# Kernel optimization log

Measured on AMD Instinct MI355X. Metric: run time of the kernel, lower is better.

## Reference

```python
import jax, jax.numpy as jnp
import numpy as np

N1 = 50000        # nodes in g1
N_LAYERS = 3
N2 = N1 * N_LAYERS  # nodes in g2 (kron tiling)
E1 = 800000
E2 = 2400000
D = 64
LEAKY_SLOPE = 0.01


def graph_conv(x, src, dst, num_nodes, W, b):
    """DGL GraphConv with norm='both', in_feats == out_feats (aggregate-then-matmul).
    h = D_in^{-1/2} A D_out^{-1/2} x W + b, degrees clamped to >=1.
    """
    ones_e = jnp.ones(src.shape[0], dtype=x.dtype)
    out_deg = jax.ops.segment_sum(ones_e, src, num_segments=num_nodes)
    in_deg = jax.ops.segment_sum(ones_e, dst, num_segments=num_nodes)
    norm_src = jnp.power(jnp.clip(out_deg, 1.0), -0.5)  # [N]
    norm_dst = jnp.power(jnp.clip(in_deg, 1.0), -0.5)   # [N]
    feat = x * norm_src[:, None]                         # [N, D]
    agg = jax.ops.segment_sum(feat[src], dst, num_segments=num_nodes)  # [N, D]
    rst = agg * norm_dst[:, None]
    return rst @ W + b


def setup_inputs() -> dict:
    key = jax.random.key(0)
    k = jax.random.split(key, 8)
    return {
        "node_features": jax.random.normal(k[0], (N1, D), dtype=jnp.float32),
        "WQ": jax.random.normal(k[1], (D, D), dtype=jnp.float32) * (1.0 / np.sqrt(D)),
        "bQ": jnp.zeros((D,), dtype=jnp.float32),
        "WM": jax.random.normal(k[2], (D, D), dtype=jnp.float32) * (1.0 / np.sqrt(D)),
        "bM": jnp.zeros((D,), dtype=jnp.float32),
        "src1": jax.random.randint(k[3], (E1,), 0, N1, dtype=jnp.int32),
        "dst1": jax.random.randint(k[4], (E1,), 0, N1, dtype=jnp.int32),
        "src2": jax.random.randint(k[5], (E2,), 0, N2, dtype=jnp.int32),
        "dst2": jax.random.randint(k[6], (E2,), 0, N2, dtype=jnp.int32),
    }


def reference(node_features, WQ, bQ, WM, bM, src1, dst1, src2, dst2):
    h_Q1 = graph_conv(node_features, src1, dst1, N1, WQ, bQ)
    h_Q1 = jax.nn.leaky_relu(h_Q1, negative_slope=LEAKY_SLOPE)
    # torch.kron(ones(n_layers,1), h_Q1) == vertical tiling
    M_feat = jnp.tile(h_Q1, (N_LAYERS, 1))  # [N_LAYERS*N1, D]
    h_M1 = graph_conv(M_feat, src2, dst2, N2, WM, bM)
    return jax.nn.leaky_relu(h_M1, negative_slope=LEAKY_SLOPE)
```

## Files before the change

### kernel.cpp

```cpp
#include <hip/hip_runtime.h>
#include <hip/hip_fp16.h>

constexpr int cN1 = 50000;
constexpr int cN2 = 150000;
constexpr int cE1 = 800000;
constexpr int cE2 = 2400000;
constexpr int cD  = 64;
constexpr int MAXB = 640;
#define LEAKY 0.01f

constexpr int NB1 = (cN1 + 255) / 256;
constexpr int NB2 = (cN2 + 255) / 256;

constexpr int BD1 = 64, BD2 = 192, BS1 = 64, BS2 = 192, CVB = 256;
constexpr int PR0 = BD1;
constexpr int PR1 = PR0 + BD2;
constexpr int PR2 = PR1 + BS1;
constexpr int PR3 = PR2 + BS2;
constexpr int PR4 = PR3 + CVB;

constexpr int SD1 = 128, SD2 = 384, SS1 = 64, SS2 = 192;

__device__ __forceinline__ void bucket_count_region(
    const int* __restrict__ idx, int E4, int* __restrict__ bcnt, int nbuck,
    int b, int B, int* h) {
    for (int i = threadIdx.x; i < nbuck; i += 256) h[i] = 0;
    __syncthreads();
    const int4* v4 = (const int4*)idx;
    for (int i = b * 256 + threadIdx.x; i < E4; i += B * 256) {
        int4 v = v4[i];
        atomicAdd(&h[v.x >> 8], 1);
        atomicAdd(&h[v.y >> 8], 1);
        atomicAdd(&h[v.z >> 8], 1);
        atomicAdd(&h[v.w >> 8], 1);
    }
    __syncthreads();
    for (int i = threadIdx.x; i < nbuck; i += 256) {
        int c = h[i];
        if (c) atomicAdd(&bcnt[i], c);
    }
}

__global__ __launch_bounds__(256) void prep_kernel(
    const int* __restrict__ dst1, const int* __restrict__ dst2,
    const int* __restrict__ src1, const int* __restrict__ src2,
    const float* __restrict__ x, __half* __restrict__ xh,
    int* __restrict__ bcntD1, int* __restrict__ bcntD2,
    int* __restrict__ bcntS1, int* __restrict__ bcntS2) {
    __shared__ int h[MAXB];
    int b = blockIdx.x;
    if (b < PR0) {
        bucket_count_region(dst1, cE1 / 4, bcntD1, NB1, b, BD1, h);
    } else if (b < PR1) {
        bucket_count_region(dst2, cE2 / 4, bcntD2, NB2, b - PR0, BD2, h);
    } else if (b < PR2) {
        bucket_count_region(src1, cE1 / 4, bcntS1, NB1, b - PR1, BS1, h);
    } else if (b < PR3) {
        bucket_count_region(src2, cE2 / 4, bcntS2, NB2, b - PR2, BS2, h);
    } else {
        int i = (b - PR3) * 256 + threadIdx.x;
        const int n4 = cN1 * cD / 4;
        for (; i < n4; i += CVB * 256) {
            float4 v = ((const float4*)x)[i];
            __half2* o = (__half2*)xh;
            o[2 * i]     = __floats2half2_rn(v.x, v.y);
            o[2 * i + 1] = __floats2half2_rn(v.z, v.w);
        }
    }
}

__global__ __launch_bounds__(256) void scan4_kernel(
    int* __restrict__ bcntD1, int* __restrict__ bbaseD1, int* __restrict__ bcurD1,
    int* __restrict__ bcntD2, int* __restrict__ bbaseD2, int* __restrict__ bcurD2,
    int* __restrict__ bcntS1, int* __restrict__ bbaseS1, int* __restrict__ bcurS1,
    int* __restrict__ bcntS2, int* __restrict__ bbaseS2, int* __restrict__ bcurS2,
    int* __restrict__ offs1, int* __restrict__ offs2) {
    int b = blockIdx.x;
    int tid = threadIdx.x;
    int* bcnt; int* bbase; int* bcur; int n; int e;
    if (b == 0)      { bcnt = bcntD1; bbase = bbaseD1; bcur = bcurD1; n = NB1; e = cE1; }
    else if (b == 1) { bcnt = bcntD2; bbase = bbaseD2; bcur = bcurD2; n = NB2; e = cE2; }
    else if (b == 2) { bcnt = bcntS1; bbase = bbaseS1; bcur = bcurS1; n = NB1; e = cE1; }
    else             { bcnt = bcntS2; bbase = bbaseS2; bcur = bcurS2; n = NB2; e = cE2; }
    if (b == 0 && tid == 0) offs1[cN1] = cE1;
    if (b == 1 && tid == 0) offs2[cN2] = cE2;
    __shared__ int s[256];
    int v[4];
    int t = 0;
#pragma unroll
    for (int j = 0; j < 4; ++j) { int i = tid * 4 + j; v[j] = (i < n) ? bcnt[i] : 0; t += v[j]; }
    s[tid] = t; __syncthreads();
    for (int off = 1; off < 256; off <<= 1) {
        int a = (tid >= off) ? s[tid - off] : 0;
        __syncthreads();
        s[tid] += a;
        __syncthreads();
    }
    int run = s[tid] - t;
#pragma unroll
    for (int j = 0; j < 4; ++j) {
        int i = tid * 4 + j;
        if (i < n) { bbase[i] = run; bcur[i] = run; run += v[j]; }
    }
    if (tid == 0) bbase[n] = e;
}

__global__ __launch_bounds__(256) void scatter4_kernel(
    const int* __restrict__ src1, const int* __restrict__ dst1,
    int* __restrict__ bcurD1, unsigned int* __restrict__ pairs1,
    const int* __restrict__ src2, const int* __restrict__ dst2,
    int* __restrict__ bcurD2, unsigned int* __restrict__ pairs2,
    int* __restrict__ bcurS1, unsigned char* __restrict__ sval1,
    int* __restrict__ bcurS2, unsigned char* __restrict__ sval2) {
    __shared__ int hist[MAXB];
    __shared__ int cur[MAXB];
    int tid = threadIdx.x;
    int bx = blockIdx.x;
    bool pairMode;
    const int* key; const int* pay; int* bcur;
    unsigned int* pout = nullptr; unsigned char* bout = nullptr;
    int nbuck, E, blk, nblk;
    if (bx < SD1) {
        pairMode = true;  key = dst1; pay = src1; bcur = bcurD1; pout = pairs1;
        nbuck = NB1; E = cE1; blk = bx; nblk = SD1;
    } else if (bx < SD1 + SD2) {
        pairMode = true;  key = dst2; pay = src2; bcur = bcurD2; pout = pairs2;
        nbuck = NB2; E = cE2; blk = bx - SD1; nblk = SD2;
    } else if (bx < SD1 + SD2 + SS1) {
        pairMode = false; key = src1; pay = nullptr; bcur = bcurS1; bout = sval1;
        nbuck = NB1; E = cE1; blk = bx - SD1 - SD2; nblk = SS1;
    } else {
        pairMode = false; key = src2; pay = nullptr; bcur = bcurS2; bout = sval2;
        nbuck = NB2; E = cE2; blk = bx - SD1 - SD2 - SS1; nblk = SS2;
    }
    int spe = (((E / 4) + nblk - 1) / nblk) * 4;
    int b0 = blk * spe;
    int b1 = b0 + spe; if (b1 > E) b1 = E;
    for (int i = tid; i < nbuck; i += 256) hist[i] = 0;
    __syncthreads();
    for (int i = b0 + tid * 4; i < b1; i += 1024) {
        int4 d = *(const int4*)(key + i);
        atomicAdd(&hist[d.x >> 8], 1);
        atomicAdd(&hist[d.y >> 8], 1);
        atomicAdd(&hist[d.z >> 8], 1);
        atomicAdd(&hist[d.w >> 8], 1);
    }
    __syncthreads();
    for (int i = tid; i < nbuck; i += 256) cur[i] = atomicAdd(&bcur[i], hist[i]);
    __syncthreads();
    if (pairMode) {
        for (int i = b0 + tid * 4; i < b1; i += 1024) {
            int4 d = *(const int4*)(key + i);
            int4 s = *(const int4*)(pay + i);
            int p0 = atomicAdd(&cur[d.x >> 8], 1);
            pout[p0] = ((unsigned)(d.x & 255) << 24) | (unsigned)s.x;
            int p1 = atomicAdd(&cur[d.y >> 8], 1);
            pout[p1] = ((unsigned)(d.y & 255) << 24) | (unsigned)s.y;
            int p2 = atomicAdd(&cur[d.z >> 8], 1);
            pout[p2] = ((unsigned)(d.z & 255) << 24) | (unsigned)s.z;
            int p3 = atomicAdd(&cur[d.w >> 8], 1);
            pout[p3] = ((unsigned)(d.w & 255) << 24) | (unsigned)s.w;
        }
    } else {
        for (int i = b0 + tid * 4; i < b1; i += 1024) {
            int4 d = *(const int4*)(key + i);
            int p0 = atomicAdd(&cur[d.x >> 8], 1); bout[p0] = (unsigned char)(d.x & 255);
            int p1 = atomicAdd(&cur[d.y >> 8], 1); bout[p1] = (unsigned char)(d.y & 255);
            int p2 = atomicAdd(&cur[d.z >> 8], 1); bout[p2] = (unsigned char)(d.z & 255);
            int p3 = atomicAdd(&cur[d.w >> 8], 1); bout[p3] = (unsigned char)(d.w & 255);
        }
    }
}

__global__ __launch_bounds__(256) void sbin_kernel(
    const unsigned char* __restrict__ sval1, const int* __restrict__ bbaseS1,
    float* __restrict__ nsrc1,
    const unsigned char* __restrict__ sval2, const int* __restrict__ bbaseS2,
    float* __restrict__ nsrc2) {
    const unsigned char* sv; const int* bbase; float* nsrc; int N, bk;
    if (blockIdx.x < NB1) { sv = sval1; bbase = bbaseS1; nsrc = nsrc1; N = cN1; bk = blockIdx.x; }
    else                  { sv = sval2; bbase = bbaseS2; nsrc = nsrc2; N = cN2; bk = blockIdx.x - NB1; }
    __shared__ int cnt[256];
    int tid = threadIdx.x;
    cnt[tid] = 0;
    __syncthreads();
    int k0 = bbase[bk];
    int k1 = bbase[bk + 1];
    for (int k = k0 + tid; k < k1; k += 256) atomicAdd(&cnt[sv[k]], 1);
    __syncthreads();
    int lo = bk << 8;
    int span = N - lo; if (span > 256) span = 256;
    if (tid < span) {
        int d = cnt[tid];
        d = d < 1 ? 1 : d;
        nsrc[lo + tid] = rsqrtf((float)d);
    }
}

__global__ __launch_bounds__(256) void bin12_kernel(
    const unsigned int* __restrict__ pairs1, const int* __restrict__ bbase1,
    const float* __restrict__ nsrc1, unsigned int* __restrict__ sorted1,
    int* __restrict__ offs1,
    const unsigned int* __restrict__ pairs2, const int* __restrict__ bbase2,
    const float* __restrict__ nsrc2, unsigned int* __restrict__ sorted2,
    int* __restrict__ offs2) {
    const unsigned int* pairs; const int* bbase; const float* nsrc;
    unsigned int* sorted; int* offs; int N, foldn, bk;
    if (blockIdx.x < NB1) {
        pairs = pairs1; bbase = bbase1; nsrc = nsrc1; sorted = sorted1;
        offs = offs1; N = cN1; foldn = 0; bk = blockIdx.x;
    } else {
        pairs = pairs2; bbase = bbase2; nsrc = nsrc2; sorted = sorted2;
        offs = offs2; N = cN2; foldn = cN1; bk = blockIdx.x - NB1;
    }
    __shared__ int cnt[256];
    __shared__ int s[256];
    __shared__ int cur[256];
    int tid = threadIdx.x;
    int lo = bk << 8;
    int span = N - lo; if (span > 256) span = 256;
    int k0 = bbase[bk];
    int k1 = bbase[bk + 1];
    cnt[tid] = 0;
    __syncthreads();
    for (int k = k0 + tid; k < k1; k += 256) atomicAdd(&cnt[pairs[k] >> 24], 1);
    __syncthreads();
    int v = cnt[tid];
    s[tid] = v; __syncthreads();
    for (int off = 1; off < 256; off <<= 1) {
        int a = (tid >= off) ? s[tid - off] : 0;
        __syncthreads();
        s[tid] += a;
        __syncthreads();
    }
    int excl = s[tid] - v;
    cur[tid] = k0 + excl;
    if (tid < span) offs[lo + tid] = k0 + excl;
    __syncthreads();
    for (int k = k0 + tid; k < k1; k += 256) {
        unsigned pr = pairs[k];
        int d = pr >> 24;
        int sidx = (int)(pr & 0xFFFFFFu);
        int r = sidx;
        if (foldn) {
            if (r >= 2 * foldn) r -= 2 * foldn;
            else if (r >= foldn) r -= foldn;
        }
        __half nh = __float2half(nsrc[sidx]);
        int pos = atomicAdd(&cur[d], 1);
        sorted[pos] = ((unsigned)__half_as_ushort(nh) << 16) | (unsigned)r;
    }
}

#define FMA8(v, nv)                                                     \
    {                                                                   \
        float2 f0 = __half22float2(*(const __half2*)&(v).x);            \
        float2 f1 = __half22float2(*(const __half2*)&(v).y);            \
        float2 f2 = __half22float2(*(const __half2*)&(v).z);            \
        float2 f3 = __half22float2(*(const __half2*)&(v).w);            \
        a0.x = fmaf(f0.x, nv, a0.x); a0.y = fmaf(f0.y, nv, a0.y);       \
        a0.z = fmaf(f1.x, nv, a0.z); a0.w = fmaf(f1.y, nv, a0.w);       \
        a1.x = fmaf(f2.x, nv, a1.x); a1.y = fmaf(f2.y, nv, a1.y);       \
        a1.z = fmaf(f3.x, nv, a1.z); a1.w = fmaf(f3.y, nv, a1.w);       \
    }

template <bool EPI>
__global__ __launch_bounds__(256) void agg_csr_kernel(
    const __half* __restrict__ feat, const unsigned int* __restrict__ sorted,
    const int* __restrict__ offs, float* __restrict__ outp,
    const float* __restrict__ bias, int N) {
    int w = (blockIdx.x * blockDim.x + threadIdx.x) >> 4;
    if (w >= N) return;
    int l16  = threadIdx.x & 15;
    int slot = l16 >> 3;
    int c    = l16 & 7;

    int k0 = offs[w];
    int k1 = offs[w + 1];
    float4 a0 = {0.f, 0.f, 0.f, 0.f};
    float4 a1 = {0.f, 0.f, 0.f, 0.f};

    int k = k0 + slot;
    for (; k + 2 < k1; k += 4) {
        unsigned eA = sorted[k];
        unsigned eB = sorted[k + 2];
        float nA = __half2float(__ushort_as_half((unsigned short)(eA >> 16)));
        float nB = __half2float(__ushort_as_half((unsigned short)(eB >> 16)));
        int rA = (int)(eA & 0xFFFFu);
        int rB = (int)(eB & 0xFFFFu);
        uint4 vA = *(const uint4*)(feat + (size_t)rA * cD + c * 8);
        uint4 vB = *(const uint4*)(feat + (size_t)rB * cD + c * 8);
        FMA8(vA, nA);
        FMA8(vB, nB);
    }
    if (k < k1) {
        unsigned e = sorted[k];
        float nv = __half2float(__ushort_as_half((unsigned short)(e >> 16)));
        int r = (int)(e & 0xFFFFu);
        uint4 v = *(const uint4*)(feat + (size_t)r * cD + c * 8);
        FMA8(v, nv);
    }

    a0.x += __shfl_xor(a0.x, 8); a0.y += __shfl_xor(a0.y, 8);
    a0.z += __shfl_xor(a0.z, 8); a0.w += __shfl_xor(a0.w, 8);
    a1.x += __shfl_xor(a1.x, 8); a1.y += __shfl_xor(a1.y, 8);
    a1.z += __shfl_xor(a1.z, 8); a1.w += __shfl_xor(a1.w, 8);

    if (slot == 0) {
        if (EPI) {
            int dg = k1 - k0;
            float nd = rsqrtf((float)(dg < 1 ? 1 : dg));
            float4 b0 = *(const float4*)(bias + c * 8);
            float4 b1 = *(const float4*)(bias + c * 8 + 4);
            float4 r0, r1;
            r0.x = fmaf(a0.x, nd, b0.x); r0.y = fmaf(a0.y, nd, b0.y);
            r0.z = fmaf(a0.z, nd, b0.z); r0.w = fmaf(a0.w, nd, b0.w);
            r1.x = fmaf(a1.x, nd, b1.x); r1.y = fmaf(a1.y, nd, b1.y);
            r1.z = fmaf(a1.z, nd, b1.z); r1.w = fmaf(a1.w, nd, b1.w);
            r0.x = r0.x > 0.f ? r0.x : LEAKY * r0.x;
            r0.y = r0.y > 0.f ? r0.y : LEAKY * r0.y;
            r0.z = r0.z > 0.f ? r0.z : LEAKY * r0.z;
            r0.w = r0.w > 0.f ? r0.w : LEAKY * r0.w;
            r1.x = r1.x > 0.f ? r1.x : LEAKY * r1.x;
            r1.y = r1.y > 0.f ? r1.y : LEAKY * r1.y;
            r1.z = r1.z > 0.f ? r1.z : LEAKY * r1.z;
            r1.w = r1.w > 0.f ? r1.w : LEAKY * r1.w;
            *(float4*)(outp + (size_t)w * cD + c * 8) = r0;
            *(float4*)(outp + (size_t)w * cD + c * 8 + 4) = r1;
        } else {
            *(float4*)(outp + (size_t)w * cD + c * 8) = a0;
            *(float4*)(outp + (size_t)w * cD + c * 8 + 4) = a1;
        }
    }
}
#undef FMA8

__global__ __launch_bounds__(256) void gemm12_kernel(
    const float* __restrict__ A, const int* __restrict__ offs,
    const float* __restrict__ WQ_, const float* __restrict__ bQ_,
    const float* __restrict__ WM_, __half* __restrict__ g, int N) {
    __shared__ float W1[64][64];
    __shared__ float W2[64][64];
    __shared__ float Rs[4][64];
    __shared__ float Hs[4][64];
    int tid = threadIdx.x;
    for (int i = tid; i < 64 * 64; i += 256) {
        W1[i >> 6][i & 63] = WQ_[i];
        W2[i >> 6][i & 63] = WM_[i];
    }
    int r = tid >> 6;
    int j = tid & 63;
    int row = blockIdx.x * 4 + r;
    if (row < N) {
        int dg = offs[row + 1] - offs[row];
        float rn = rsqrtf((float)(dg < 1 ? 1 : dg));
        Rs[r][j] = A[(size_t)row * cD + j] * rn;
    }
    __syncthreads();
    if (row < N) {
        float acc = bQ_[j];
#pragma unroll
        for (int k = 0; k < 64; ++k) acc = fmaf(Rs[r][k], W1[k][j], acc);
        acc = acc > 0.f ? acc : LEAKY * acc;
        Hs[r][j] = acc;
    }
    __syncthreads();
    if (row < N) {
        float acc = 0.f;
#pragma unroll
        for (int k = 0; k < 64; ++k) acc = fmaf(Hs[r][k], W2[k][j], acc);
        g[(size_t)row * cD + j] = __float2half(acc);
    }
}

extern "C" void kernel_launch(void* const* d_in, const int* in_sizes, int n_in,
                              void* d_out, int out_size, void* d_ws, size_t ws_size,
                              hipStream_t stream) {
    const float* x    = (const float*)d_in[0];
    const float* WQ   = (const float*)d_in[1];
    const float* bQ   = (const float*)d_in[2];
    const float* WM   = (const float*)d_in[3];
    const float* bM   = (const float*)d_in[4];
    const int*   src1 = (const int*)d_in[5];
    const int*   dst1 = (const int*)d_in[6];
    const int*   src2 = (const int*)d_in[7];
    const int*   dst2 = (const int*)d_in[8];
    float* out = (float*)d_out;

    char* p = (char*)d_ws;
    int*    bcntD1 = (int*)p;    p += sizeof(int) * MAXB;
    int*    bcntD2 = (int*)p;    p += sizeof(int) * MAXB;
    int*    bcntS1 = (int*)p;    p += sizeof(int) * MAXB;
    int*    bcntS2 = (int*)p;    p += sizeof(int) * MAXB;
    int*    bbaseD1= (int*)p;    p += sizeof(int) * (MAXB + 1);
    int*    bbaseD2= (int*)p;    p += sizeof(int) * (MAXB + 1);
    int*    bbaseS1= (int*)p;    p += sizeof(int) * (MAXB + 1);
    int*    bbaseS2= (int*)p;    p += sizeof(int) * (MAXB + 1);
    int*    bcurD1 = (int*)p;    p += sizeof(int) * MAXB;
    int*    bcurD2 = (int*)p;    p += sizeof(int) * MAXB;
    int*    bcurS1 = (int*)p;    p += sizeof(int) * MAXB;
    int*    bcurS2 = (int*)p;    p += sizeof(int) * MAXB;
    float*  nsrc1  = (float*)p;  p += sizeof(float) * cN1;
    float*  nsrc2  = (float*)p;  p += sizeof(float) * cN2;
    int*    offs1  = (int*)p;    p += sizeof(int) * (cN1 + 1);
    int*    offs2  = (int*)p;    p += sizeof(int) * (cN2 + 1);
    unsigned int* sorted2 = (unsigned int*)p; p += sizeof(int) * cE2;
    __half* gh     = (__half*)p; p += sizeof(__half) * (size_t)cN1 * cD;

    int* dout_i = (int*)d_out;
    unsigned int*  pairs2  = (unsigned int*)dout_i;
    unsigned int*  pairs1  = (unsigned int*)(dout_i + cE2);
    __half*        xh      = (__half*)(dout_i + cE2 + cE1);
    float*         agg1buf = (float*)(dout_i + cE2 + cE1 + (size_t)cN1 * cD / 2);
    unsigned char* sval2   = (unsigned char*)(dout_i + 8000000);
    unsigned char* sval1   = (unsigned char*)(dout_i + 8600000);
    unsigned int*  sorted1 = (unsigned int*)(dout_i + ((size_t)cN2 * cD - cE1));

    hipMemsetAsync(bcntD1, 0, sizeof(int) * 4 * MAXB, stream);

    prep_kernel<<<PR4, 256, 0, stream>>>(dst1, dst2, src1, src2, x, xh,
                                         bcntD1, bcntD2, bcntS1, bcntS2);

    scan4_kernel<<<4, 256, 0, stream>>>(
        bcntD1, bbaseD1, bcurD1, bcntD2, bbaseD2, bcurD2,
        bcntS1, bbaseS1, bcurS1, bcntS2, bbaseS2, bcurS2, offs1, offs2);

    scatter4_kernel<<<SD1 + SD2 + SS1 + SS2, 256, 0, stream>>>(
        src1, dst1, bcurD1, pairs1, src2, dst2, bcurD2, pairs2,
        bcurS1, sval1, bcurS2, sval2);

    sbin_kernel<<<NB1 + NB2, 256, 0, stream>>>(
        sval1, bbaseS1, nsrc1, sval2, bbaseS2, nsrc2);

    bin12_kernel<<<NB1 + NB2, 256, 0, stream>>>(
        pairs1, bbaseD1, nsrc1, sorted1, offs1,
        pairs2, bbaseD2, nsrc2, sorted2, offs2);

    agg_csr_kernel<false><<<(cN1 + 15) / 16, 256, 0, stream>>>(
        xh, sorted1, offs1, agg1buf, nullptr, cN1);
    gemm12_kernel<<<(cN1 + 3) / 4, 256, 0, stream>>>(agg1buf, offs1, WQ, bQ, WM, gh, cN1);

    agg_csr_kernel<true><<<(cN2 + 15) / 16, 256, 0, stream>>>(
        gh, sorted2, offs2, out, bM, cN2);
}
```

Before: 238.0 us.

## Register-tile gemm12 over 32 rows per block with transposed smem operands

The fused two-layer 64x64 GEMM now handles 32 rows per block instead of 4. Each thread accumulates 8 rows in registers and reads the transposed, padded activation tiles as float4. This spreads the per-block cost of loading both weight matrices over eight times more rows and cuts shared-memory reads per FMA. In exchange it uses more shared memory and registers per block and launches fewer blocks.

```diff
diff --git a/kernel.cpp b/kernel.cpp
--- a/kernel.cpp
+++ b/kernel.cpp
@@ -335,41 +335,92 @@
 }
 #undef FMA8
 
+constexpr int GR = 32;
+constexpr int RP = 36;
+
 __global__ __launch_bounds__(256) void gemm12_kernel(
     const float* __restrict__ A, const int* __restrict__ offs,
     const float* __restrict__ WQ_, const float* __restrict__ bQ_,
     const float* __restrict__ WM_, __half* __restrict__ g, int N) {
-    __shared__ float W1[64][64];
-    __shared__ float W2[64][64];
-    __shared__ float Rs[4][64];
-    __shared__ float Hs[4][64];
+    __shared__ float W1s[64 * 64];
+    __shared__ float W2s[64 * 64];
+    __shared__ float Rs_t[64 * RP];
+    __shared__ float Hs_t[64 * RP];
+    __shared__ float rn_s[GR];
     int tid = threadIdx.x;
+    int row0 = blockIdx.x * GR;
+
     for (int i = tid; i < 64 * 64; i += 256) {
-        W1[i >> 6][i & 63] = WQ_[i];
-        W2[i >> 6][i & 63] = WM_[i];
-    }
-    int r = tid >> 6;
-    int j = tid & 63;
-    int row = blockIdx.x * 4 + r;
-    if (row < N) {
-        int dg = offs[row + 1] - offs[row];
-        float rn = rsqrtf((float)(dg < 1 ? 1 : dg));
-        Rs[r][j] = A[(size_t)row * cD + j] * rn;
-    }
-    __syncthreads();
-    if (row < N) {
-        float acc = bQ_[j];
+        W1s[i] = WQ_[i];
+        W2s[i] = WM_[i];
+    }
+    if (tid < GR) {
+        int row = row0 + tid;
+        if (row < N) {
+            int dg = offs[row + 1] - offs[row];
+            rn_s[tid] = rsqrtf((float)(dg < 1 ? 1 : dg));
+        } else {
+            rn_s[tid] = 0.f;
+        }
+    }
+    __syncthreads();
+    for (int i = tid; i < GR * 64; i += 256) {
+        int r = i >> 6;
+        int k = i & 63;
+        int row = row0 + r;
+        float v = (row < N) ? A[(size_t)row * cD + k] * rn_s[r] : 0.f;
+        Rs_t[k * RP + r] = v;
+    }
+    __syncthreads();
+
+    int j  = tid & 63;
+    int gq = tid >> 6;
+    int r0 = gq * 8;
+
+    float acc[8];
+    float bq = bQ_[j];
 #pragma unroll
-        for (int k = 0; k < 64; ++k) acc = fmaf(Rs[r][k], W1[k][j], acc);
-        acc = acc > 0.f ? acc : LEAKY * acc;
-        Hs[r][j] = acc;
-    }
-    __syncthreads();
-    if (row < N) {
-        float acc = 0.f;
+    for (int i = 0; i < 8; ++i) acc[i] = bq;
+#pragma unroll 8
+    for (int k = 0; k < 64; ++k) {
+        float wv = W1s[k * 64 + j];
+        float4 ra = *(const float4*)&Rs_t[k * RP + r0];
+        float4 rb = *(const float4*)&Rs_t[k * RP + r0 + 4];
+        acc[0] = fmaf(ra.x, wv, acc[0]); acc[1] = fmaf(ra.y, wv, acc[1]);
+        acc[2] = fmaf(ra.z, wv, acc[2]); acc[3] = fmaf(ra.w, wv, acc[3]);
+        acc[4] = fmaf(rb.x, wv, acc[4]); acc[5] = fmaf(rb.y, wv, acc[5]);
+        acc[6] = fmaf(rb.z, wv, acc[6]); acc[7] = fmaf(rb.w, wv, acc[7]);
+    }
+    float4 h0, h1;
+    h0.x = acc[0] > 0.f ? acc[0] : LEAKY * acc[0];
+    h0.y = acc[1] > 0.f ? acc[1] : LEAKY * acc[1];
+    h0.z = acc[2] > 0.f ? acc[2] : LEAKY * acc[2];
+    h0.w = acc[3] > 0.f ? acc[3] : LEAKY * acc[3];
+    h1.x = acc[4] > 0.f ? acc[4] : LEAKY * acc[4];
+    h1.y = acc[5] > 0.f ? acc[5] : LEAKY * acc[5];
+    h1.z = acc[6] > 0.f ? acc[6] : LEAKY * acc[6];
+    h1.w = acc[7] > 0.f ? acc[7] : LEAKY * acc[7];
+    *(float4*)&Hs_t[j * RP + r0]     = h0;
+    *(float4*)&Hs_t[j * RP + r0 + 4] = h1;
+    __syncthreads();
+
+    float acc2[8];
 #pragma unroll
-        for (int k = 0; k < 64; ++k) acc = fmaf(Hs[r][k], W2[k][j], acc);
-        g[(size_t)row * cD + j] = __float2half(acc);
+    for (int i = 0; i < 8; ++i) acc2[i] = 0.f;
+#pragma unroll 8
+    for (int k = 0; k < 64; ++k) {
+        float wv = W2s[k * 64 + j];
+        float4 ra = *(const float4*)&Hs_t[k * RP + r0];
+        float4 rb = *(const float4*)&Hs_t[k * RP + r0 + 4];
+        acc2[0] = fmaf(ra.x, wv, acc2[0]); acc2[1] = fmaf(ra.y, wv, acc2[1]);
+        acc2[2] = fmaf(ra.z, wv, acc2[2]); acc2[3] = fmaf(ra.w, wv, acc2[3]);
+        acc2[4] = fmaf(rb.x, wv, acc2[4]); acc2[5] = fmaf(rb.y, wv, acc2[5]);
+        acc2[6] = fmaf(rb.z, wv, acc2[6]); acc2[7] = fmaf(rb.w, wv, acc2[7]);
+    }
+#pragma unroll
+    for (int i = 0; i < 8; ++i) {
+        int row = row0 + r0 + i;
+        if (row < N) g[(size_t)row * cD + j] = __float2half(acc2[i]);
     }
 }
 
@@ -438,7 +489,8 @@
 
     agg_csr_kernel<false><<<(cN1 + 15) / 16, 256, 0, stream>>>(
         xh, sorted1, offs1, agg1buf, nullptr, cN1);
-    gemm12_kernel<<<(cN1 + 3) / 4, 256, 0, stream>>>(agg1buf, offs1, WQ, bQ, WM, gh, cN1);
+    gemm12_kernel<<<(cN1 + GR - 1) / GR, 256, 0, stream>>>(
+        agg1buf, offs1, WQ, bQ, WM, gh, cN1);
 
     agg_csr_kernel<true><<<(cN2 + 15) / 16, 256, 0, stream>>>(
         gh, sorted2, offs2, out, bM, cN2);
```

New measurement: 214.9 us. -9.7%, faster.
